# Kernel tuning notes

Hardware: AMD Instinct MI355X
Metric: run time of the kernel (lower is better)

The kernel has to match this reference:

```python
import jax, jax.numpy as jnp
import numpy as np


def segment_pool(labels, hidden):
    """Faithful vectorized version of get_entity_embedding_from_hidden_states.

    labels: [B, L] int (0=O, 1=B, 2=I); hidden: [B, L, H].
    Returns [B, L, H]: per-row, the first count_ones(row) slots hold the mean
    hidden state of each mention segment (segments delimited by label==1 over
    the nonzero-label token stream, flattened across the whole batch), rest 0.
    """
    B, L, H = hidden.shape
    N = B * L
    lab = labels.reshape(N)
    h = hidden.reshape(N, H)
    m = lab != 0
    # stable sort: nonzero-label tokens first, original order preserved
    perm = jnp.argsort(jnp.logical_not(m))
    lab_s = lab[perm]
    h_s = h[perm]
    m_s = m[perm]
    b = (lab_s == 1).astype(jnp.int32)
    cum = jnp.cumsum(b)                      # ones seen so far (nonzero stream)
    idx0 = jnp.argmax(b)                     # position of first B-tag (0 if none)
    p = jnp.arange(N)
    # chunk id of nonzero-stream token p: (#ones at positions <= p+idx0) - 1
    seg = cum[jnp.minimum(p + idx0, N - 1)] - 1
    valid = m_s & (seg >= 0)
    seg_ids = jnp.where(valid, seg, N)       # invalid tokens -> dumped segment N
    sums = jax.ops.segment_sum(h_s, seg_ids, num_segments=N + 1)[:N]
    counts = jax.ops.segment_sum(valid.astype(h.dtype), seg_ids, num_segments=N + 1)[:N]
    means = sums / jnp.maximum(counts, 1.0)[:, None]   # [N, H]
    # re-split per row: row b consumes count_ones(b) consecutive means, padded to L
    c = jnp.sum(labels == 1, axis=1)         # [B]
    starts = jnp.cumsum(c) - c               # exclusive prefix sum
    j = jnp.arange(L)
    gidx = jnp.clip(starts[:, None] + j[None, :], 0, N - 1)  # [B, L]
    out = means[gidx]                        # [B, L, H]
    return jnp.where((j[None, :] < c[:, None])[:, :, None], out, jnp.zeros((), hidden.dtype))


def setup_inputs() -> dict:
    key = jax.random.key(0)
    ks = jax.random.split(key, 8)
    B, L, H, E, P = 64, 512, 768, 1000, 300
    return {
        "bio_slot_labels": jax.random.randint(ks[0], (B, L), 0, 3, dtype=jnp.int32),
        "hidden_states": jax.random.normal(ks[1], (B, L, H), dtype=jnp.float32),
        "entity_type_embeddings": jax.random.normal(ks[2], (E, H), dtype=jnp.float32),
        "w1": jax.random.normal(ks[3], (H, H), dtype=jnp.float32) * 0.02,
        "b1": jnp.zeros((H,), dtype=jnp.float32),
        "w2": jax.random.normal(ks[4], (H, 3), dtype=jnp.float32) * 0.02,
        "b2": jnp.zeros((3,), dtype=jnp.float32),
        "w_mention": jax.random.normal(ks[5], (H, P), dtype=jnp.float32) * 0.02,
        "w_desc": jax.random.normal(ks[6], (H, P), dtype=jnp.float32) * 0.02,
    }


def reference(bio_slot_labels, hidden_states, entity_type_embeddings,
              w1, b1, w2, b2, w_mention, w_desc):
    # bio_mlp: Linear -> ReLU -> Linear -> LogSoftmax
    h1 = jax.nn.relu(jnp.einsum('blh,hk->blk', hidden_states, w1) + b1)
    bio_slot_logits = jax.nn.log_softmax(jnp.einsum('blh,hc->blc', h1, w2) + b2, axis=-1)
    predicted_bio_slot = jnp.argmax(bio_slot_logits, axis=-1)

    proj_desc = entity_type_embeddings @ w_desc          # [E, 300]

    def score(labels):
        pooled = segment_pool(labels, hidden_states)     # [B, L, H]
        proj_mention = jnp.einsum('blh,hp->blp', pooled, w_mention)
        dot = jnp.einsum('blp,ep->ble', proj_mention, proj_desc)
        return jax.nn.log_softmax(dot, axis=-1)

    return (bio_slot_logits, score(bio_slot_labels), score(predicted_bio_slot))
```

## Files before the change

kernel.cpp:

```cpp
#include <hip/hip_runtime.h>
#include <stdint.h>

__device__ inline float bf2f(unsigned short u) { return __uint_as_float(((unsigned int)u) << 16); }
__device__ inline unsigned short f2bf(float f) {
    unsigned int x = __float_as_uint(f);
    unsigned int r = x + 0x7fffu + ((x >> 16) & 1u);
    return (unsigned short)(r >> 16);
}

typedef __attribute__((ext_vector_type(8))) short bf16x8;
typedef __attribute__((ext_vector_type(4))) float f32x4;
typedef __attribute__((ext_vector_type(4))) int   v4i;
typedef __attribute__((ext_vector_type(4))) unsigned short u16x4;

#define FLAG_CAP 8192
#define MARGIN 0.02

__global__ __launch_bounds__(256) void gemm_bt(
    const unsigned short* __restrict__ A,
    const unsigned short* __restrict__ Bt,
    void* __restrict__ C,
    const int* __restrict__ Mdev,
    const int* __restrict__ rowMap,
    const float* __restrict__ fb1,
    const float* __restrict__ fw2,
    float* __restrict__ fpart,
    int M, int N, int K, int lda, int ldb, int ldc, int mode, int rowOff)
{
    if (Mdev) M = *Mdev;
    int nt = blockIdx.x, mt = blockIdx.y;
    if (rowOff + mt * 128 >= M) return;

    __shared__ __align__(16) unsigned short As[128 * 64];
    __shared__ __align__(16) unsigned short Bs[128 * 64];

    int tid  = threadIdx.x;
    int lane = tid & 63, wave = tid >> 6;
    int wRow = (wave >> 1) * 64, wCol = (wave & 1) * 64;
    int mBase = mt * 128, nBase = nt * 128;
    int lm = lane & 15, kg = lane >> 4;
    int sr = tid >> 3;
    int sc = (tid & 7) * 8;

    f32x4 acc[4][4] = {};

    for (int k0 = 0; k0 < K; k0 += 64) {
        __syncthreads();
#pragma unroll
        for (int i = 0; i < 4; ++i) {
            int r = sr + 32 * i;
            int gm = rowOff + mBase + r; if (gm > M - 1) gm = M - 1;
            *(v4i*)&As[r * 64 + sc] = *(const v4i*)&A[(size_t)(gm - rowOff) * lda + k0 + sc];
            int gn = nBase + r; if (gn > N - 1) gn = N - 1;
            *(v4i*)&Bs[r * 64 + sc] = *(const v4i*)&Bt[(size_t)gn * ldb + k0 + sc];
        }
        __syncthreads();
#pragma unroll
        for (int ks = 0; ks < 2; ++ks) {
            bf16x8 af[4], bfr[4];
#pragma unroll
            for (int i = 0; i < 4; ++i) {
                af[i]  = *(const bf16x8*)&As[(wRow + i * 16 + lm) * 64 + ks * 32 + kg * 8];
                bfr[i] = *(const bf16x8*)&Bs[(wCol + i * 16 + lm) * 64 + ks * 32 + kg * 8];
            }
#pragma unroll
            for (int mi = 0; mi < 4; ++mi)
#pragma unroll
                for (int ni = 0; ni < 4; ++ni)
                    acc[mi][ni] = __builtin_amdgcn_mfma_f32_16x16x32_bf16(
                        af[mi], bfr[ni], acc[mi][ni], 0, 0, 0);
        }
    }

    int rbase = (lane >> 4) * 4;

    if (mode == 3) {
        float b1v[4], w2l[4][3];
#pragma unroll
        for (int ni = 0; ni < 4; ++ni) {
            int n = nBase + wCol + ni * 16 + lm;
            b1v[ni] = fb1[n];
#pragma unroll
            for (int c = 0; c < 3; ++c) w2l[ni][c] = fw2[n * 3 + c];
        }
#pragma unroll
        for (int mi = 0; mi < 4; ++mi) {
            float p[4][3] = {};
#pragma unroll
            for (int ni = 0; ni < 4; ++ni)
#pragma unroll
                for (int r = 0; r < 4; ++r) {
                    float v = acc[mi][ni][r] + b1v[ni];
                    v = fmaxf(v, 0.f);
                    p[r][0] += v * w2l[ni][0];
                    p[r][1] += v * w2l[ni][1];
                    p[r][2] += v * w2l[ni][2];
                }
#pragma unroll
            for (int r = 0; r < 4; ++r)
#pragma unroll
                for (int c = 0; c < 3; ++c) {
                    float s = p[r][c];
                    s += __shfl_down(s, 8); s += __shfl_down(s, 4);
                    s += __shfl_down(s, 2); s += __shfl_down(s, 1);
                    p[r][c] = s;
                }
            if (lm == 0) {
#pragma unroll
                for (int r = 0; r < 4; ++r) {
                    int row = mBase + wRow + mi * 16 + rbase + r;
#pragma unroll
                    for (int c = 0; c < 3; ++c)
                        atomicAdd(&fpart[(size_t)row * 3 + c], p[r][c]);
                }
            }
        }
        return;
    }

#pragma unroll
    for (int mi = 0; mi < 4; ++mi) {
#pragma unroll
        for (int r = 0; r < 4; ++r) {
            int m = rowOff + mBase + wRow + mi * 16 + rbase + r;
            if (m >= M) continue;
            size_t crow = rowMap ? (size_t)rowMap[m] * ldc : (size_t)(m - rowOff) * ldc;
#pragma unroll
            for (int ni = 0; ni < 4; ++ni) {
                int n = nBase + wCol + ni * 16 + lm;
                if (n >= N) continue;
                float v = acc[mi][ni][r];
                if (mode == 2) ((float*)C)[crow + n] = v;
                else           ((unsigned short*)C)[crow + n] = f2bf(v);
            }
        }
    }
}

__global__ void cast_bf16_v4(const float* __restrict__ in, unsigned short* __restrict__ out,
                             int n4)
{
    int i = blockIdx.x * 256 + threadIdx.x;
    if (i < n4) {
        float4 v = ((const float4*)in)[i];
        u16x4 o = { f2bf(v.x), f2bf(v.y), f2bf(v.z), f2bf(v.w) };
        ((u16x4*)out)[i] = o;
    }
}

__global__ void cast_pad(const float* __restrict__ in, unsigned short* __restrict__ out,
                         int rows, int cols, int ldo)
{
    int idx = blockIdx.x * 256 + threadIdx.x;
    if (idx < rows * cols) out[(size_t)(idx / cols) * ldo + (idx % cols)] = f2bf(in[idx]);
}

__global__ void transpose_cast(const float* __restrict__ in, unsigned short* __restrict__ out,
                               int R, int Ccols)
{
    __shared__ float tile[32][33];
    int c0 = blockIdx.x * 32, r0 = blockIdx.y * 32;
    int tx = threadIdx.x, ty = threadIdx.y;
#pragma unroll
    for (int i = 0; i < 4; ++i) {
        int r = r0 + ty + i * 8, c = c0 + tx;
        if (r < R && c < Ccols) tile[ty + i * 8][tx] = in[(size_t)r * Ccols + c];
    }
    __syncthreads();
#pragma unroll
    for (int i = 0; i < 4; ++i) {
        int orow = c0 + ty + i * 8;
        int ocol = r0 + tx;
        if (orow < Ccols && ocol < R) out[(size_t)orow * R + ocol] = f2bf(tile[tx][ty + i * 8]);
    }
}

__global__ void bio_final2(const float* __restrict__ part, const float* __restrict__ b2,
                           float* __restrict__ out0, int* __restrict__ predLab,
                           int* __restrict__ flagCnt, int* __restrict__ flagList)
{
    int t = blockIdx.x * 256 + threadIdx.x;
    double a[3];
#pragma unroll
    for (int c = 0; c < 3; ++c) a[c] = (double)part[(size_t)t * 3 + c] + (double)b2[c];
    double mx = a[0]; if (a[1] > mx) mx = a[1]; if (a[2] > mx) mx = a[2];
    double ls = mx + log(exp(a[0] - mx) + exp(a[1] - mx) + exp(a[2] - mx));
    out0[t * 3 + 0] = (float)(a[0] - ls);
    out0[t * 3 + 1] = (float)(a[1] - ls);
    out0[t * 3 + 2] = (float)(a[2] - ls);
    int pbest = 0; double bv = a[0];
    if (a[1] > bv) { bv = a[1]; pbest = 1; }
    if (a[2] > bv) { bv = a[2]; pbest = 2; }
    predLab[t] = pbest;
    double second = -1e300;
#pragma unroll
    for (int c = 0; c < 3; ++c) if (c != pbest && a[c] > second) second = a[c];
    if (bv - second < MARGIN) {
        int i = atomicAdd(flagCnt, 1);
        if (i < FLAG_CAP) flagList[i] = t;
    }
}

__global__ void gather_rows(const float* __restrict__ A, const int* __restrict__ flagList,
                            const int* __restrict__ flagCnt, float* __restrict__ Af)
{
    int b = blockIdx.x;
    int cnt = *flagCnt; if (cnt > FLAG_CAP) cnt = FLAG_CAP;
    if (b >= cnt) return;
    const float* src = A + (size_t)flagList[b] * 768;
    float* dst = Af + (size_t)b * 768;
    int t = threadIdx.x;
    dst[t] = src[t]; dst[t + 256] = src[t + 256]; dst[t + 512] = src[t + 512];
}

__global__ __launch_bounds__(256) void h1_bio_gemm(
    const float* __restrict__ A, const float* __restrict__ W,
    const float* __restrict__ b1, const float* __restrict__ w2,
    float* __restrict__ part, const int* __restrict__ Mdev, int partStride)
{
    int M = *Mdev; if (M > FLAG_CAP) M = FLAG_CAP;
    if (M <= 0) return;
    int m0 = blockIdx.x * 64, n0 = blockIdx.y * 64;
    if (m0 >= M) return;
    __shared__ float AsT[16][64];
    __shared__ float Ws[16][64];
    int tx = threadIdx.x, ty = threadIdx.y;
    int tid = ty * 16 + tx;
    float acc[4][4] = {};

    for (int k0 = 0; k0 < 768; k0 += 16) {
        __syncthreads();
        {
            int row = tid >> 2, seg = (tid & 3) * 4;
            int gm = m0 + row; if (gm > M - 1) gm = M - 1;
            float4 v = *(const float4*)&A[(size_t)gm * 768 + k0 + seg];
            AsT[seg + 0][row] = v.x; AsT[seg + 1][row] = v.y;
            AsT[seg + 2][row] = v.z; AsT[seg + 3][row] = v.w;
        }
        {
            int row = tid >> 4, seg = (tid & 15) * 4;
            *(float4*)&Ws[row][seg] = *(const float4*)&W[(size_t)(k0 + row) * 768 + n0 + seg];
        }
        __syncthreads();
#pragma unroll
        for (int kk = 0; kk < 16; ++kk) {
            float4 av = *(const float4*)&AsT[kk][ty * 4];
            float4 bv = *(const float4*)&Ws[kk][tx * 4];
            float a[4] = {av.x, av.y, av.z, av.w};
            float b[4] = {bv.x, bv.y, bv.z, bv.w};
#pragma unroll
            for (int i = 0; i < 4; ++i)
#pragma unroll
                for (int j = 0; j < 4; ++j)
                    acc[i][j] += a[i] * b[j];
        }
    }

    float b1v[4], w2l[4][3];
#pragma unroll
    for (int j = 0; j < 4; ++j) {
        int n = n0 + tx * 4 + j;
        b1v[j] = b1[n];
#pragma unroll
        for (int c = 0; c < 3; ++c) w2l[j][c] = w2[n * 3 + c];
    }
    float p[4][3] = {};
#pragma unroll
    for (int i = 0; i < 4; ++i)
#pragma unroll
        for (int j = 0; j < 4; ++j) {
            float v = acc[i][j] + b1v[j];
            v = fmaxf(v, 0.f);
#pragma unroll
            for (int c = 0; c < 3; ++c) p[i][c] += v * w2l[j][c];
        }
#pragma unroll
    for (int i = 0; i < 4; ++i)
#pragma unroll
        for (int c = 0; c < 3; ++c) {
            float s = p[i][c];
            s += __shfl_down(s, 8); s += __shfl_down(s, 4);
            s += __shfl_down(s, 2); s += __shfl_down(s, 1);
            p[i][c] = s;
        }
    if (tx == 0) {
#pragma unroll
        for (int i = 0; i < 4; ++i) {
            int t = m0 + ty * 4 + i;
            if (t >= M) continue;
#pragma unroll
            for (int c = 0; c < 3; ++c)
                part[(size_t)blockIdx.y * partStride + (size_t)t * 3 + c] = p[i][c];
        }
    }
}

__global__ void bio_final_fix(const float* __restrict__ partF, const float* __restrict__ b2,
                              const int* __restrict__ flagList, const int* __restrict__ flagCnt,
                              int* __restrict__ predLab, int partStride)
{
    int i = blockIdx.x * 256 + threadIdx.x;
    int cnt = *flagCnt; if (cnt > FLAG_CAP) cnt = FLAG_CAP;
    if (i >= cnt) return;
    double a[3] = {(double)b2[0], (double)b2[1], (double)b2[2]};
#pragma unroll
    for (int blk = 0; blk < 12; ++blk)
#pragma unroll
        for (int c = 0; c < 3; ++c)
            a[c] += (double)partF[(size_t)blk * partStride + (size_t)i * 3 + c];
    int pbest = 0; double bv = a[0];
    if (a[1] > bv) { bv = a[1]; pbest = 1; }
    if (a[2] > bv) { bv = a[2]; pbest = 2; }
    predLab[flagList[i]] = pbest;
}

__global__ void seg_init(int* segCount, int* segFirst)
{
    int i = blockIdx.x * 256 + threadIdx.x;
    segCount[i] = 0;
    segFirst[i] = 0x7fffffff;
}

__global__ __launch_bounds__(1024) void seg_prep(
    const int* __restrict__ lab, int* __restrict__ streamTok, int* __restrict__ cumArr,
    int* __restrict__ meta, int* __restrict__ rowC, int* __restrict__ rowStart,
    int* __restrict__ mapArr)
{
    __shared__ int sM[1024], sB[1024];
    __shared__ int sRowC[64], sRowStart[64];
    __shared__ int sIdx0;
    int t = threadIdx.x;
    if (t == 0) sIdx0 = 0x7fffffff;
    int base = t * 32;
    int mc = 0, bc = 0;
    for (int i = 0; i < 32; ++i) { int v = lab[base + i]; mc += (v != 0); bc += (v == 1); }
    sM[t] = mc; sB[t] = bc; __syncthreads();
    for (int off = 1; off < 1024; off <<= 1) {
        int vm = 0, vb = 0;
        if (t >= off) { vm = sM[t - off]; vb = sB[t - off]; }
        __syncthreads();
        sM[t] += vm; sB[t] += vb;
        __syncthreads();
    }
    int mBase = sM[t] - mc, bBase = sB[t] - bc;
    int mRun = 0, bRun = 0;
    for (int i = 0; i < 32; ++i) {
        int v = lab[base + i];
        if (v != 0) {
            int q = mBase + mRun;
            streamTok[q] = base + i;
            int isB = (v == 1);
            cumArr[q] = bBase + bRun + isB;
            if (isB && (bBase + bRun) == 0) sIdx0 = q;
            mRun += 1; bRun += isB;
        }
    }
    if ((t & 15) == 0) sRowStart[t >> 4] = bBase;
    __syncthreads();
    if ((t & 15) == 0) {
        int b = t >> 4;
        sRowC[b] = sB[t + 15] - sRowStart[b];
        rowStart[b] = sRowStart[b];
        rowC[b] = sRowC[b];
    }
    if (t == 1023) { meta[0] = sB[1023]; meta[1] = sM[1023]; }
    if (t == 0) meta[2] = (sIdx0 == 0x7fffffff) ? 0 : sIdx0;
    __syncthreads();
    for (int idx = t; idx < 32768; idx += 1024) {
        int b = idx >> 9, j = idx & 511;
        if (j < sRowC[b]) mapArr[sRowStart[b] + j] = idx;
    }
}

__global__ void seg_assign(const int* __restrict__ cumArr, int* __restrict__ segCount,
                           int* __restrict__ segFirst, const int* __restrict__ meta)
{
    int q = blockIdx.x * 256 + threadIdx.x;
    int K = meta[1];
    if (q >= K) return;
    int numB = meta[0], idx0 = meta[2];
    int qq = q + idx0;
    int cumv = (qq < K) ? cumArr[qq] : numB;
    int seg = cumv - 1;
    if (seg >= 0) {
        atomicAdd(&segCount[seg], 1);
        atomicMin(&segFirst[seg], q);
    }
}

__global__ __launch_bounds__(256) void seg_means(
    const unsigned short* __restrict__ hiddenB, const int* __restrict__ streamTok,
    const int* __restrict__ segCount, const int* __restrict__ segFirst,
    const int* __restrict__ meta, unsigned short* __restrict__ means, int s0)
{
    int s = s0 + blockIdx.x;
    if (s >= meta[0]) return;
    int t = threadIdx.x;
    float a0 = 0.f, a1 = 0.f, a2 = 0.f;
    int cnt = segCount[s];
    if (cnt > 0) {
        int q0 = segFirst[s];
        for (int i = 0; i < cnt; ++i) {
            const unsigned short* hr = hiddenB + (size_t)streamTok[q0 + i] * 768;
            a0 += bf2f(hr[t]); a1 += bf2f(hr[t + 256]); a2 += bf2f(hr[t + 512]);
        }
        float fc = (float)cnt;
        a0 /= fc; a1 /= fc; a2 /= fc;
    }
    size_t o = (size_t)(s - s0) * 768;
    means[o + t] = f2bf(a0); means[o + t + 256] = f2bf(a1); means[o + t + 512] = f2bf(a2);
}

__global__ __launch_bounds__(256) void softmax_rows(float* __restrict__ out,
                                                    const int* __restrict__ rowC)
{
    int v = blockIdx.x;
    int b = v >> 9, j = v & 511;
    int t = threadIdx.x;
    float* row = out + (size_t)v * 1000;
    if (j >= rowC[b]) {
        for (int e = t; e < 1000; e += 256) row[e] = -6.907755278982137f;
        return;
    }
    __shared__ float red[256];
    float x0 = row[t];
    float x1 = row[t + 256];
    float x2 = row[t + 512];
    bool has3 = (t + 768) < 1000;
    float x3 = has3 ? row[t + 768] : -1e30f;
    float mx = fmaxf(fmaxf(x0, x1), fmaxf(x2, x3));
    red[t] = mx; __syncthreads();
    for (int st = 128; st > 0; st >>= 1) { if (t < st) red[t] = fmaxf(red[t], red[t + st]); __syncthreads(); }
    float M = red[0]; __syncthreads();
    float sm = expf(x0 - M) + expf(x1 - M) + expf(x2 - M) + (has3 ? expf(x3 - M) : 0.f);
    red[t] = sm; __syncthreads();
    for (int st = 128; st > 0; st >>= 1) { if (t < st) red[t] += red[t + st]; __syncthreads(); }
    float ls = M + logf(red[0]);
    row[t]       = x0 - ls;
    row[t + 256] = x1 - ls;
    row[t + 512] = x2 - ls;
    if (has3) row[t + 768] = x3 - ls;
}

extern "C" void kernel_launch(void* const* d_in, const int* in_sizes, int n_in,
                              void* d_out, int out_size, void* d_ws, size_t ws_size,
                              hipStream_t stream)
{
    (void)in_sizes; (void)n_in; (void)out_size; (void)ws_size;
    const int*   labels = (const int*)d_in[0];
    const float* hidden = (const float*)d_in[1];
    const float* ent    = (const float*)d_in[2];
    const float* w1     = (const float*)d_in[3];
    const float* b1     = (const float*)d_in[4];
    const float* w2     = (const float*)d_in[5];
    const float* b2     = (const float*)d_in[6];
    const float* wm     = (const float*)d_in[7];
    const float* wd     = (const float*)d_in[8];

    char* ws = (char*)d_ws;
    size_t off = 0;
    auto alloc = [&](size_t bytes) {
        void* p = ws + off;
        off = (off + bytes + 255) & ~(size_t)255;
        return p;
    };
    int* meta      = (int*)alloc(256);
    int* rowC      = (int*)alloc(256);
    int* rowStart  = (int*)alloc(256);
    int* flagCnt   = (int*)alloc(256);
    int* predLab   = (int*)alloc(32768 * 4);
    int* streamTok = (int*)alloc(32768 * 4);
    int* cumArr    = (int*)alloc(32768 * 4);
    int* segCount  = (int*)alloc(32768 * 4);
    int* segFirst  = (int*)alloc(32768 * 4);
    int* mapArr    = (int*)alloc(32768 * 4);
    int* flagList  = (int*)alloc(FLAG_CAP * 4);
    unsigned short* entB = (unsigned short*)alloc((size_t)1000 * 768 * 2);
    unsigned short* wdT  = (unsigned short*)alloc((size_t)300 * 768 * 2);
    unsigned short* pd   = (unsigned short*)alloc((size_t)1000 * 320 * 2);
    unsigned short* wmP  = (unsigned short*)alloc((size_t)768 * 320 * 2);
    unsigned short* W2t  = (unsigned short*)alloc((size_t)1000 * 768 * 2);
    unsigned short* w1T  = (unsigned short*)alloc((size_t)768 * 768 * 2);
    unsigned short* hiddenB = (unsigned short*)alloc((size_t)32768 * 768 * 2);
    float* part  = (float*)alloc((size_t)32768 * 3 * 4);
    float* partF = (float*)alloc((size_t)12 * FLAG_CAP * 3 * 4);
    float* Af    = (float*)alloc((size_t)FLAG_CAP * 768 * 4);
    unsigned short* meansChunk = (unsigned short*)alloc((size_t)8192 * 768 * 2);

    float* out0 = (float*)d_out;
    float* out1 = out0 + 98304;
    float* out2 = out1 + (size_t)32768 * 1000;

    hipMemsetAsync(pd, 0, (size_t)1000 * 320 * 2, stream);
    hipMemsetAsync(wmP, 0, (size_t)768 * 320 * 2, stream);
    hipMemsetAsync(part, 0, (size_t)32768 * 3 * 4, stream);
    hipMemsetAsync(flagCnt, 0, 4, stream);
    cast_bf16_v4<<<750, 256, 0, stream>>>(ent, entB, 192000);
    cast_bf16_v4<<<24576, 256, 0, stream>>>(hidden, hiddenB, 6291456);
    transpose_cast<<<dim3(10, 24), dim3(32, 8), 0, stream>>>(wd, wdT, 768, 300);
    transpose_cast<<<dim3(24, 24), dim3(32, 8), 0, stream>>>(w1, w1T, 768, 768);
    cast_pad<<<900, 256, 0, stream>>>(wm, wmP, 768, 300, 320);
    gemm_bt<<<dim3(3, 8), 256, 0, stream>>>(entB, wdT, pd, nullptr, nullptr,
                                            nullptr, nullptr, nullptr,
                                            1000, 300, 768, 768, 768, 320, 0, 0);
    gemm_bt<<<dim3(6, 8), 256, 0, stream>>>(pd, wmP, W2t, nullptr, nullptr,
                                            nullptr, nullptr, nullptr,
                                            1000, 768, 320, 320, 320, 768, 0, 0);

    gemm_bt<<<dim3(6, 256), 256, 0, stream>>>(hiddenB, w1T, nullptr, nullptr, nullptr,
                                              b1, w2, part,
                                              32768, 768, 768, 768, 768, 0, 3, 0);
    bio_final2<<<128, 256, 0, stream>>>(part, b2, out0, predLab, flagCnt, flagList);
    gather_rows<<<FLAG_CAP, 256, 0, stream>>>(hidden, flagList, flagCnt, Af);
    h1_bio_gemm<<<dim3(FLAG_CAP / 64, 12), dim3(16, 16), 0, stream>>>(
        Af, w1, b1, w2, partF, flagCnt, FLAG_CAP * 3);
    bio_final_fix<<<FLAG_CAP / 256, 256, 0, stream>>>(partF, b2, flagList, flagCnt,
                                                      predLab, FLAG_CAP * 3);

    for (int s = 0; s < 2; ++s) {
        const int* lab = (s == 0) ? labels : predLab;
        float* outS = (s == 0) ? out1 : out2;
        seg_init<<<128, 256, 0, stream>>>(segCount, segFirst);
        seg_prep<<<1, 1024, 0, stream>>>(lab, streamTok, cumArr, meta, rowC, rowStart, mapArr);
        seg_assign<<<128, 256, 0, stream>>>(cumArr, segCount, segFirst, meta);
        for (int c = 0; c < 4; ++c) {
            int s0 = c * 8192;
            seg_means<<<8192, 256, 0, stream>>>(hiddenB, streamTok, segCount, segFirst,
                                                meta, meansChunk, s0);
            gemm_bt<<<dim3(8, 64), 256, 0, stream>>>(meansChunk, W2t, outS, meta, mapArr,
                                                     nullptr, nullptr, nullptr,
                                                     0, 1000, 768, 768, 768, 1000, 2, s0);
        }
        softmax_rows<<<32768, 256, 0, stream>>>(outS, rowC);
    }
}
```

Before: 932.4 us.

## Batch both scoring passes into single launches and fuse prep kernels

Fuses the casts, transposes, padding and memsets into one prep kernel. Both label sets now run segmentation, means, the score GEMM and the softmax together through grid z/y dimensions instead of a host loop of chunked launches. Segment boundaries are found by neighbour comparison rather than atomics, and the flagged-row gather is folded into the fallback GEMM. The GEMM tile loads now use global_load_lds direct-to-LDS copies. Together these cut launch count and serialization, at the cost of a much larger means buffer.

```diff
diff --git a/kernel.cpp b/kernel.cpp
--- a/kernel.cpp
+++ b/kernel.cpp
@@ -15,6 +15,12 @@
 
 #define FLAG_CAP 8192
 #define MARGIN 0.02
+
+__device__ inline void gload16(const void* g, void* l) {
+    __builtin_amdgcn_global_load_lds(
+        (const __attribute__((address_space(1))) void*)g,
+        (__attribute__((address_space(3))) void*)l, 16, 0, 0);
+}
 
 __global__ __launch_bounds__(256) void gemm_bt(
     const unsigned short* __restrict__ A,
@@ -25,9 +31,14 @@
     const float* __restrict__ fb1,
     const float* __restrict__ fw2,
     float* __restrict__ fpart,
-    int M, int N, int K, int lda, int ldb, int ldc, int mode, int rowOff)
-{
-    if (Mdev) M = *Mdev;
+    int M, int N, int K, int lda, int ldb, int ldc, int mode, int rowOff,
+    size_t zA, int zMeta, int zMap, size_t zC)
+{
+    int zz = blockIdx.z;
+    A += (size_t)zz * zA;
+    if (Mdev) M = Mdev[zz * zMeta];
+    if (rowMap) rowMap += (size_t)zz * zMap;
+
     int nt = blockIdx.x, mt = blockIdx.y;
     if (rowOff + mt * 128 >= M) return;
 
@@ -50,9 +61,9 @@
         for (int i = 0; i < 4; ++i) {
             int r = sr + 32 * i;
             int gm = rowOff + mBase + r; if (gm > M - 1) gm = M - 1;
-            *(v4i*)&As[r * 64 + sc] = *(const v4i*)&A[(size_t)(gm - rowOff) * lda + k0 + sc];
+            gload16(&A[(size_t)(gm - rowOff) * lda + k0 + sc], &As[wave * 512 + i * 2048]);
             int gn = nBase + r; if (gn > N - 1) gn = N - 1;
-            *(v4i*)&Bs[r * 64 + sc] = *(const v4i*)&Bt[(size_t)gn * ldb + k0 + sc];
+            gload16(&Bt[(size_t)gn * ldb + k0 + sc], &Bs[wave * 512 + i * 2048]);
         }
         __syncthreads();
 #pragma unroll
@@ -130,48 +141,68 @@
                 int n = nBase + wCol + ni * 16 + lm;
                 if (n >= N) continue;
                 float v = acc[mi][ni][r];
-                if (mode == 2) ((float*)C)[crow + n] = v;
+                if (mode == 2) ((float*)C)[(size_t)zz * zC + crow + n] = v;
                 else           ((unsigned short*)C)[crow + n] = f2bf(v);
             }
         }
     }
 }
 
-__global__ void cast_bf16_v4(const float* __restrict__ in, unsigned short* __restrict__ out,
-                             int n4)
-{
-    int i = blockIdx.x * 256 + threadIdx.x;
-    if (i < n4) {
-        float4 v = ((const float4*)in)[i];
+__global__ __launch_bounds__(256) void prep_all(
+    const float* __restrict__ ent, unsigned short* __restrict__ entB,
+    const float* __restrict__ hidden, unsigned short* __restrict__ hiddenB,
+    const float* __restrict__ wd, unsigned short* __restrict__ wdT,
+    const float* __restrict__ w1, unsigned short* __restrict__ w1T,
+    const float* __restrict__ wm, unsigned short* __restrict__ wmP,
+    v4i* __restrict__ zreg)
+{
+    __shared__ float tile[32][33];
+    int b = blockIdx.x, t = threadIdx.x;
+    if (b < 373) {
+        int i = b * 256 + t;
+        if (i < 95312) { v4i z = {0, 0, 0, 0}; zreg[i] = z; }
+        return;
+    }
+    b -= 373;
+    if (b < 750) {
+        int i = b * 256 + t;
+        float4 v = ((const float4*)ent)[i];
         u16x4 o = { f2bf(v.x), f2bf(v.y), f2bf(v.z), f2bf(v.w) };
-        ((u16x4*)out)[i] = o;
-    }
-}
-
-__global__ void cast_pad(const float* __restrict__ in, unsigned short* __restrict__ out,
-                         int rows, int cols, int ldo)
-{
-    int idx = blockIdx.x * 256 + threadIdx.x;
-    if (idx < rows * cols) out[(size_t)(idx / cols) * ldo + (idx % cols)] = f2bf(in[idx]);
-}
-
-__global__ void transpose_cast(const float* __restrict__ in, unsigned short* __restrict__ out,
-                               int R, int Ccols)
-{
-    __shared__ float tile[32][33];
-    int c0 = blockIdx.x * 32, r0 = blockIdx.y * 32;
-    int tx = threadIdx.x, ty = threadIdx.y;
-#pragma unroll
-    for (int i = 0; i < 4; ++i) {
-        int r = r0 + ty + i * 8, c = c0 + tx;
-        if (r < R && c < Ccols) tile[ty + i * 8][tx] = in[(size_t)r * Ccols + c];
-    }
-    __syncthreads();
-#pragma unroll
-    for (int i = 0; i < 4; ++i) {
-        int orow = c0 + ty + i * 8;
-        int ocol = r0 + tx;
-        if (orow < Ccols && ocol < R) out[(size_t)orow * R + ocol] = f2bf(tile[tx][ty + i * 8]);
+        ((u16x4*)entB)[i] = o;
+        return;
+    }
+    b -= 750;
+    if (b < 24576) {
+        int i = b * 256 + t;
+        float4 v = ((const float4*)hidden)[i];
+        u16x4 o = { f2bf(v.x), f2bf(v.y), f2bf(v.z), f2bf(v.w) };
+        ((u16x4*)hiddenB)[i] = o;
+        return;
+    }
+    b -= 24576;
+    if (b < 240 + 576) {
+        const float* in; unsigned short* out; int R, C, bx, by;
+        if (b < 240) { in = wd; out = wdT; R = 768; C = 300; bx = b % 10; by = b / 10; }
+        else { int bb = b - 240; in = w1; out = w1T; R = 768; C = 768; bx = bb % 24; by = bb / 24; }
+        int tx = t & 31, ty = t >> 5;
+        int c0 = bx * 32, r0 = by * 32;
+#pragma unroll
+        for (int i = 0; i < 4; ++i) {
+            int r = r0 + ty + i * 8, c = c0 + tx;
+            if (r < R && c < C) tile[ty + i * 8][tx] = in[(size_t)r * C + c];
+        }
+        __syncthreads();
+#pragma unroll
+        for (int i = 0; i < 4; ++i) {
+            int orow = c0 + ty + i * 8, ocol = r0 + tx;
+            if (orow < C && ocol < R) out[(size_t)orow * R + ocol] = f2bf(tile[tx][ty + i * 8]);
+        }
+        return;
+    }
+    b -= 816;
+    {
+        int idx = b * 256 + t;
+        if (idx < 768 * 300) wmP[(size_t)(idx / 300) * 320 + (idx % 300)] = f2bf(wm[idx]);
     }
 }
 
@@ -201,20 +232,9 @@
     }
 }
 
-__global__ void gather_rows(const float* __restrict__ A, const int* __restrict__ flagList,
-                            const int* __restrict__ flagCnt, float* __restrict__ Af)
-{
-    int b = blockIdx.x;
-    int cnt = *flagCnt; if (cnt > FLAG_CAP) cnt = FLAG_CAP;
-    if (b >= cnt) return;
-    const float* src = A + (size_t)flagList[b] * 768;
-    float* dst = Af + (size_t)b * 768;
-    int t = threadIdx.x;
-    dst[t] = src[t]; dst[t + 256] = src[t + 256]; dst[t + 512] = src[t + 512];
-}
-
 __global__ __launch_bounds__(256) void h1_bio_gemm(
-    const float* __restrict__ A, const float* __restrict__ W,
+    const float* __restrict__ hidden, const int* __restrict__ flagList,
+    const float* __restrict__ W,
     const float* __restrict__ b1, const float* __restrict__ w2,
     float* __restrict__ part, const int* __restrict__ Mdev, int partStride)
 {
@@ -233,7 +253,7 @@
         {
             int row = tid >> 2, seg = (tid & 3) * 4;
             int gm = m0 + row; if (gm > M - 1) gm = M - 1;
-            float4 v = *(const float4*)&A[(size_t)gm * 768 + k0 + seg];
+            float4 v = *(const float4*)&hidden[(size_t)flagList[gm] * 768 + k0 + seg];
             AsT[seg + 0][row] = v.x; AsT[seg + 1][row] = v.y;
             AsT[seg + 2][row] = v.z; AsT[seg + 3][row] = v.w;
         }
@@ -314,26 +334,35 @@
     predLab[flagList[i]] = pbest;
 }
 
-__global__ void seg_init(int* segCount, int* segFirst)
-{
-    int i = blockIdx.x * 256 + threadIdx.x;
-    segCount[i] = 0;
-    segFirst[i] = 0x7fffffff;
-}
-
-__global__ __launch_bounds__(1024) void seg_prep(
-    const int* __restrict__ lab, int* __restrict__ streamTok, int* __restrict__ cumArr,
-    int* __restrict__ meta, int* __restrict__ rowC, int* __restrict__ rowStart,
-    int* __restrict__ mapArr)
-{
+__global__ __launch_bounds__(1024) void seg_prep2(
+    const int* __restrict__ labels, const int* __restrict__ predLab,
+    int* __restrict__ streamTok, int* __restrict__ cumArr,
+    int* __restrict__ meta, int* __restrict__ rowC, int* __restrict__ mapArr)
+{
+    int setz = blockIdx.x;
+    const int* lab = setz ? predLab : labels;
+    int* sTok = streamTok + setz * 32768;
+    int* sCum = cumArr + setz * 32768;
+    int* mt   = meta + setz * 64;
+    int* rC   = rowC + setz * 64;
+    int* mp   = mapArr + setz * 32768;
+
     __shared__ int sM[1024], sB[1024];
     __shared__ int sRowC[64], sRowStart[64];
     __shared__ int sIdx0;
     int t = threadIdx.x;
     if (t == 0) sIdx0 = 0x7fffffff;
     int base = t * 32;
+    int vals[32];
+#pragma unroll
+    for (int j = 0; j < 8; ++j) {
+        v4i v = ((const v4i*)lab)[t * 8 + j];
+        vals[4 * j + 0] = v[0]; vals[4 * j + 1] = v[1];
+        vals[4 * j + 2] = v[2]; vals[4 * j + 3] = v[3];
+    }
     int mc = 0, bc = 0;
-    for (int i = 0; i < 32; ++i) { int v = lab[base + i]; mc += (v != 0); bc += (v == 1); }
+#pragma unroll
+    for (int i = 0; i < 32; ++i) { mc += (vals[i] != 0); bc += (vals[i] == 1); }
     sM[t] = mc; sB[t] = bc; __syncthreads();
     for (int off = 1; off < 1024; off <<= 1) {
         int vm = 0, vb = 0;
@@ -344,13 +373,14 @@
     }
     int mBase = sM[t] - mc, bBase = sB[t] - bc;
     int mRun = 0, bRun = 0;
+#pragma unroll
     for (int i = 0; i < 32; ++i) {
-        int v = lab[base + i];
+        int v = vals[i];
         if (v != 0) {
             int q = mBase + mRun;
-            streamTok[q] = base + i;
+            sTok[q] = base + i;
             int isB = (v == 1);
-            cumArr[q] = bBase + bRun + isB;
+            sCum[q] = bBase + bRun + isB;
             if (isB && (bBase + bRun) == 0) sIdx0 = q;
             mRun += 1; bRun += isB;
         }
@@ -360,60 +390,74 @@
     if ((t & 15) == 0) {
         int b = t >> 4;
         sRowC[b] = sB[t + 15] - sRowStart[b];
-        rowStart[b] = sRowStart[b];
-        rowC[b] = sRowC[b];
-    }
-    if (t == 1023) { meta[0] = sB[1023]; meta[1] = sM[1023]; }
-    if (t == 0) meta[2] = (sIdx0 == 0x7fffffff) ? 0 : sIdx0;
+        rC[b] = sRowC[b];
+    }
+    if (t == 1023) { mt[0] = sB[1023]; mt[1] = sM[1023]; }
+    if (t == 0) mt[2] = (sIdx0 == 0x7fffffff) ? 0 : sIdx0;
     __syncthreads();
     for (int idx = t; idx < 32768; idx += 1024) {
         int b = idx >> 9, j = idx & 511;
-        if (j < sRowC[b]) mapArr[sRowStart[b] + j] = idx;
-    }
-}
-
-__global__ void seg_assign(const int* __restrict__ cumArr, int* __restrict__ segCount,
-                           int* __restrict__ segFirst, const int* __restrict__ meta)
-{
+        if (j < sRowC[b]) mp[sRowStart[b] + j] = idx;
+    }
+}
+
+__global__ void seg_bound(const int* __restrict__ cumArr, int* __restrict__ segFirst,
+                          const int* __restrict__ meta)
+{
+    int setz = blockIdx.y;
+    const int* cum = cumArr + setz * 32768;
+    int* sf = segFirst + setz * 32768;
+    const int* mt = meta + setz * 64;
     int q = blockIdx.x * 256 + threadIdx.x;
-    int K = meta[1];
+    int K = mt[1];
     if (q >= K) return;
-    int numB = meta[0], idx0 = meta[2];
+    int numB = mt[0], idx0 = mt[2];
     int qq = q + idx0;
-    int cumv = (qq < K) ? cumArr[qq] : numB;
-    int seg = cumv - 1;
-    if (seg >= 0) {
-        atomicAdd(&segCount[seg], 1);
-        atomicMin(&segFirst[seg], q);
-    }
-}
-
-__global__ __launch_bounds__(256) void seg_means(
+    int c  = (qq < K) ? cum[qq] : numB;
+    int sg = c - 1;
+    if (sg < 0) return;
+    int sp = -1;
+    if (q > 0) {
+        int qq2 = qq - 1;
+        int c2  = (qq2 < K) ? cum[qq2] : numB;
+        sp = c2 - 1;
+    }
+    if (sg != sp) sf[sg] = q;
+}
+
+__global__ __launch_bounds__(256) void seg_means2(
     const unsigned short* __restrict__ hiddenB, const int* __restrict__ streamTok,
-    const int* __restrict__ segCount, const int* __restrict__ segFirst,
-    const int* __restrict__ meta, unsigned short* __restrict__ means, int s0)
-{
-    int s = s0 + blockIdx.x;
-    if (s >= meta[0]) return;
+    const int* __restrict__ segFirst, const int* __restrict__ meta,
+    unsigned short* __restrict__ means, size_t zMeans)
+{
+    int setz = blockIdx.y;
+    const int* mt = meta + setz * 64;
+    int s = blockIdx.x;
+    int numB = mt[0];
+    if (s >= numB) return;
+    const int* st = streamTok + setz * 32768;
+    const int* sf = segFirst + setz * 32768;
+    int q0 = sf[s];
+    int q1 = (s + 1 < numB) ? sf[s + 1] : mt[1];
+    int cnt = q1 - q0;
     int t = threadIdx.x;
     float a0 = 0.f, a1 = 0.f, a2 = 0.f;
-    int cnt = segCount[s];
-    if (cnt > 0) {
-        int q0 = segFirst[s];
-        for (int i = 0; i < cnt; ++i) {
-            const unsigned short* hr = hiddenB + (size_t)streamTok[q0 + i] * 768;
-            a0 += bf2f(hr[t]); a1 += bf2f(hr[t + 256]); a2 += bf2f(hr[t + 512]);
-        }
-        float fc = (float)cnt;
-        a0 /= fc; a1 /= fc; a2 /= fc;
-    }
-    size_t o = (size_t)(s - s0) * 768;
-    means[o + t] = f2bf(a0); means[o + t + 256] = f2bf(a1); means[o + t + 512] = f2bf(a2);
-}
-
-__global__ __launch_bounds__(256) void softmax_rows(float* __restrict__ out,
-                                                    const int* __restrict__ rowC)
-{
+    for (int i = 0; i < cnt; ++i) {
+        const unsigned short* hr = hiddenB + (size_t)st[q0 + i] * 768;
+        a0 += bf2f(hr[t]); a1 += bf2f(hr[t + 256]); a2 += bf2f(hr[t + 512]);
+    }
+    float fc = (float)cnt;
+    a0 /= fc; a1 /= fc; a2 /= fc;
+    unsigned short* o = means + (size_t)setz * zMeans + (size_t)s * 768;
+    o[t] = f2bf(a0); o[t + 256] = f2bf(a1); o[t + 512] = f2bf(a2);
+}
+
+__global__ __launch_bounds__(256) void softmax_rows2(float* __restrict__ outBase,
+                                                     const int* __restrict__ rowCBase,
+                                                     size_t zC)
+{
+    float* out = outBase + (size_t)blockIdx.y * zC;
+    const int* rowC = rowCBase + blockIdx.y * 64;
     int v = blockIdx.x;
     int b = v >> 9, j = v & 511;
     int t = threadIdx.x;
@@ -464,73 +508,60 @@
         off = (off + bytes + 255) & ~(size_t)255;
         return p;
     };
-    int* meta      = (int*)alloc(256);
-    int* rowC      = (int*)alloc(256);
-    int* rowStart  = (int*)alloc(256);
-    int* flagCnt   = (int*)alloc(256);
+    int* meta      = (int*)alloc(512);
+    int* rowC      = (int*)alloc(512);
     int* predLab   = (int*)alloc(32768 * 4);
-    int* streamTok = (int*)alloc(32768 * 4);
-    int* cumArr    = (int*)alloc(32768 * 4);
-    int* segCount  = (int*)alloc(32768 * 4);
-    int* segFirst  = (int*)alloc(32768 * 4);
-    int* mapArr    = (int*)alloc(32768 * 4);
+    int* streamTok = (int*)alloc(2 * 32768 * 4);
+    int* cumArr    = (int*)alloc(2 * 32768 * 4);
+    int* segFirst  = (int*)alloc(2 * 32768 * 4);
+    int* mapArr    = (int*)alloc(2 * 32768 * 4);
     int* flagList  = (int*)alloc(FLAG_CAP * 4);
     unsigned short* entB = (unsigned short*)alloc((size_t)1000 * 768 * 2);
     unsigned short* wdT  = (unsigned short*)alloc((size_t)300 * 768 * 2);
-    unsigned short* pd   = (unsigned short*)alloc((size_t)1000 * 320 * 2);
-    unsigned short* wmP  = (unsigned short*)alloc((size_t)768 * 320 * 2);
     unsigned short* W2t  = (unsigned short*)alloc((size_t)1000 * 768 * 2);
     unsigned short* w1T  = (unsigned short*)alloc((size_t)768 * 768 * 2);
     unsigned short* hiddenB = (unsigned short*)alloc((size_t)32768 * 768 * 2);
-    float* part  = (float*)alloc((size_t)32768 * 3 * 4);
     float* partF = (float*)alloc((size_t)12 * FLAG_CAP * 3 * 4);
-    float* Af    = (float*)alloc((size_t)FLAG_CAP * 768 * 4);
-    unsigned short* meansChunk = (unsigned short*)alloc((size_t)8192 * 768 * 2);
+    char* zbase = (char*)alloc(1524992);
+    unsigned short* pd  = (unsigned short*)zbase;
+    unsigned short* wmP = (unsigned short*)(zbase + 640000);
+    float* part         = (float*)(zbase + 1131520);
+    int* flagCnt        = (int*)(zbase + 1524736);
+    unsigned short* means = (unsigned short*)alloc((size_t)2 * 32768 * 768 * 2);
 
     float* out0 = (float*)d_out;
     float* out1 = out0 + 98304;
-    float* out2 = out1 + (size_t)32768 * 1000;
-
-    hipMemsetAsync(pd, 0, (size_t)1000 * 320 * 2, stream);
-    hipMemsetAsync(wmP, 0, (size_t)768 * 320 * 2, stream);
-    hipMemsetAsync(part, 0, (size_t)32768 * 3 * 4, stream);
-    hipMemsetAsync(flagCnt, 0, 4, stream);
-    cast_bf16_v4<<<750, 256, 0, stream>>>(ent, entB, 192000);
-    cast_bf16_v4<<<24576, 256, 0, stream>>>(hidden, hiddenB, 6291456);
-    transpose_cast<<<dim3(10, 24), dim3(32, 8), 0, stream>>>(wd, wdT, 768, 300);
-    transpose_cast<<<dim3(24, 24), dim3(32, 8), 0, stream>>>(w1, w1T, 768, 768);
-    cast_pad<<<900, 256, 0, stream>>>(wm, wmP, 768, 300, 320);
+
+    prep_all<<<27415, 256, 0, stream>>>(ent, entB, hidden, hiddenB, wd, wdT,
+                                        w1, w1T, wm, wmP, (v4i*)zbase);
+
     gemm_bt<<<dim3(3, 8), 256, 0, stream>>>(entB, wdT, pd, nullptr, nullptr,
                                             nullptr, nullptr, nullptr,
-                                            1000, 300, 768, 768, 768, 320, 0, 0);
+                                            1000, 300, 768, 768, 768, 320, 0, 0,
+                                            0, 0, 0, 0);
     gemm_bt<<<dim3(6, 8), 256, 0, stream>>>(pd, wmP, W2t, nullptr, nullptr,
                                             nullptr, nullptr, nullptr,
-                                            1000, 768, 320, 320, 320, 768, 0, 0);
+                                            1000, 768, 320, 320, 320, 768, 0, 0,
+                                            0, 0, 0, 0);
 
     gemm_bt<<<dim3(6, 256), 256, 0, stream>>>(hiddenB, w1T, nullptr, nullptr, nullptr,
                                               b1, w2, part,
-                                              32768, 768, 768, 768, 768, 0, 3, 0);
+                                              32768, 768, 768, 768, 768, 0, 3, 0,
+                                              0, 0, 0, 0);
     bio_final2<<<128, 256, 0, stream>>>(part, b2, out0, predLab, flagCnt, flagList);
-    gather_rows<<<FLAG_CAP, 256, 0, stream>>>(hidden, flagList, flagCnt, Af);
     h1_bio_gemm<<<dim3(FLAG_CAP / 64, 12), dim3(16, 16), 0, stream>>>(
-        Af, w1, b1, w2, partF, flagCnt, FLAG_CAP * 3);
+        hidden, flagList, w1, b1, w2, partF, flagCnt, FLAG_CAP * 3);
     bio_final_fix<<<FLAG_CAP / 256, 256, 0, stream>>>(partF, b2, flagList, flagCnt,
                                                       predLab, FLAG_CAP * 3);
 
-    for (int s = 0; s < 2; ++s) {
-        const int* lab = (s == 0) ? labels : predLab;
-        float* outS = (s == 0) ? out1 : out2;
-        seg_init<<<128, 256, 0, stream>>>(segCount, segFirst);
-        seg_prep<<<1, 1024, 0, stream>>>(lab, streamTok, cumArr, meta, rowC, rowStart, mapArr);
-        seg_assign<<<128, 256, 0, stream>>>(cumArr, segCount, segFirst, meta);
-        for (int c = 0; c < 4; ++c) {
-            int s0 = c * 8192;
-            seg_means<<<8192, 256, 0, stream>>>(hiddenB, streamTok, segCount, segFirst,
-                                                meta, meansChunk, s0);
-            gemm_bt<<<dim3(8, 64), 256, 0, stream>>>(meansChunk, W2t, outS, meta, mapArr,
-                                                     nullptr, nullptr, nullptr,
-                                                     0, 1000, 768, 768, 768, 1000, 2, s0);
-        }
-        softmax_rows<<<32768, 256, 0, stream>>>(outS, rowC);
-    }
-}
+    seg_prep2<<<2, 1024, 0, stream>>>(labels, predLab, streamTok, cumArr, meta, rowC, mapArr);
+    seg_bound<<<dim3(128, 2), 256, 0, stream>>>(cumArr, segFirst, meta);
+    seg_means2<<<dim3(32768, 2), 256, 0, stream>>>(hiddenB, streamTok, segFirst, meta,
+                                                   means, (size_t)32768 * 768);
+    gemm_bt<<<dim3(8, 256, 2), 256, 0, stream>>>(means, W2t, out1, meta, mapArr,
+                                                 nullptr, nullptr, nullptr,
+                                                 0, 1000, 768, 768, 768, 1000, 2, 0,
+                                                 (size_t)32768 * 768, 64, 32768,
+                                                 (size_t)32768 * 1000);
+    softmax_rows2<<<dim3(32768, 2), 256, 0, stream>>>(out1, rowC, (size_t)32768 * 1000);
+}
```

After: 789.1 us. -15.4%, faster.
